# Performance work log

Measured on AMD Instinct MI355X. Metric: run time of the kernel, lower is better.

The kernel has to match this reference:

```python
import jax, jax.numpy as jnp
import numpy as np

N_NODES = 10000
N_EDGES = 640000
D = 128            # node_dims == edge_dims
HID = 2 * D        # ff hidden
EPS = 1e-6


def _layernorm(x, g, b):
    mu = jnp.mean(x, axis=-1, keepdims=True)
    var = jnp.var(x, axis=-1, keepdims=True)
    return (x - mu) * jax.lax.rsqrt(var + EPS) * g + b


def setup_inputs() -> dict:
    key = jax.random.key(0)
    ks = jax.random.split(key, 16)
    def lin(k, fan_in, fan_out):
        lim = 1.0 / np.sqrt(fan_in)
        kw, kb = jax.random.split(k)
        W = jax.random.uniform(kw, (fan_in, fan_out), jnp.float32, -lim, lim)
        b = jax.random.uniform(kb, (fan_out,), jnp.float32, -lim, lim)
        return W, b
    x = jax.random.normal(ks[0], (N_NODES, D), jnp.float32)
    edge_index = jax.random.randint(ks[1], (2, N_EDGES), 0, N_NODES, jnp.int64)
    edge_attr = jax.random.normal(ks[2], (N_EDGES, D), jnp.float32)
    # message MLP: Linear(3D->D), ReLU, Linear(D->D), ReLU, Linear(D->D)
    W1, b1 = lin(ks[3], 3 * D, D)
    W2, b2 = lin(ks[4], D, D)
    W3, b3 = lin(ks[5], D, D)
    # feedforward: Linear(D->2D), ReLU, Linear(2D->D)
    F1, bf1 = lin(ks[6], D, HID)
    F2, bf2 = lin(ks[7], HID, D)
    g0 = jnp.ones((D,), jnp.float32); be0 = jnp.zeros((D,), jnp.float32)
    g1 = jnp.ones((D,), jnp.float32); be1 = jnp.zeros((D,), jnp.float32)
    return {"x": x, "edge_index": edge_index, "edge_attr": edge_attr,
            "W1": W1, "b1": b1, "W2": W2, "b2": b2, "W3": W3, "b3": b3,
            "F1": F1, "bf1": bf1, "F2": F2, "bf2": bf2,
            "g0": g0, "be0": be0, "g1": g1, "be1": be1}


def reference(x, edge_index, edge_attr, W1, b1, W2, b2, W3, b3,
              F1, bf1, F2, bf2, g0, be0, g1, be1):
    src = edge_index[0]  # j
    dst = edge_index[1]  # i
    # message: cat([h_V_i, edge_attr, h_V_j]) -> MLP  (E x 3D gather)
    m = jnp.concatenate([x[dst], edge_attr, x[src]], axis=-1)
    m = jax.nn.relu(m @ W1 + b1)
    m = jax.nn.relu(m @ W2 + b2)
    m = m @ W3 + b3  # [E, D]
    # scatter-mean over destination nodes
    sums = jax.ops.segment_sum(m, dst, num_segments=N_NODES)
    cnt = jax.ops.segment_sum(jnp.ones((N_EDGES,), m.dtype), dst, num_segments=N_NODES)
    dh = sums / jnp.maximum(cnt, 1.0)[:, None]
    # residual + norm (dropout is identity at inference)
    h = _layernorm(x + dh, g0, be0)
    # pointwise feedforward
    ff = jax.nn.relu(h @ F1 + bf1) @ F2 + bf2
    return _layernorm(h + ff, g1, be1)
```

## Files before the change

kernel.cpp:

```cpp
#include <hip/hip_runtime.h>


#define NE 640000
#define NN 10000
#define DD 128
#define HIDN 256
#define EPSF 1e-6f

typedef __attribute__((ext_vector_type(8))) short short8;
typedef __attribute__((ext_vector_type(4))) float f32x4;

__device__ __forceinline__ unsigned short f2bf(float f) {
    union { float f; unsigned int u; } v; v.f = f;
    unsigned int r = v.u + 0x7FFFu + ((v.u >> 16) & 1u);
    return (unsigned short)(r >> 16);
}
__device__ __forceinline__ float bf2f(unsigned short h) {
    union { unsigned int u; float f; } v; v.u = ((unsigned int)h) << 16;
    return v.f;
}

__global__ void prep_weights(const float* __restrict__ W1,
                             const float* __restrict__ W2,
                             const float* __restrict__ W3,
                             unsigned short* __restrict__ WT)
{
    int g = blockIdx.x * 256 + threadIdx.x;
    int layer = g >> 14, r = g & 16383;
    int n = r >> 7, k = r & 127;
    const float* W = (layer == 0) ? (W1 + 128 * DD) : (layer == 1 ? W2 : W3);
    WT[layer * 16384 + n * 128 + ((((k >> 3) ^ (n & 7)) << 3) | (k & 7))] =
        f2bf(W[k * DD + n]);
}

__global__ __launch_bounds__(256, 2)
void pq_kernel(const float* __restrict__ x, const float* __restrict__ W1,
               const float* __restrict__ b1,
               unsigned short* __restrict__ Pb, unsigned short* __restrict__ Qb)
{
    __shared__ float sXT[128 * 68];
    __shared__ float sB[32 * 128];
    const int t = threadIdx.x;
    const int nb = blockIdx.x * 64;
    const int r0 = (t >> 4) << 2, c0 = (t & 15) << 3;

#pragma unroll
    for (int p = 0; p < 8; ++p) {
        int f = t + p * 256;
        int row = f >> 5, c4 = (f & 31) << 2;
        int node = nb + row; if (node >= NN) node = NN - 1;
        float4 v = *(const float4*)(x + (long)node * DD + c4);
        sXT[(c4 + 0) * 68 + row] = v.x;
        sXT[(c4 + 1) * 68 + row] = v.y;
        sXT[(c4 + 2) * 68 + row] = v.z;
        sXT[(c4 + 3) * 68 + row] = v.w;
    }

    for (int pass = 0; pass < 2; ++pass) {
        const float* W = W1 + (pass == 0 ? 0 : 256 * DD);
        float acc[4][8];
#pragma unroll
        for (int i = 0; i < 4; ++i)
#pragma unroll
            for (int j = 0; j < 8; ++j) acc[i][j] = 0.f;

        for (int kc = 0; kc < 4; ++kc) {
            __syncthreads();
#pragma unroll
            for (int p = 0; p < 4; ++p) {
                int f = t + p * 256;
                int kr = f >> 5, col = (f & 31) << 2;
                *(float4*)(sB + kr * 128 + col) =
                    *(const float4*)(W + (long)(kc * 32 + kr) * DD + col);
            }
            __syncthreads();
#pragma unroll 4
            for (int k = 0; k < 32; ++k) {
                float4 a  = *(const float4*)(sXT + (kc * 32 + k) * 68 + r0);
                float4 bl = *(const float4*)(sB + k * 128 + c0);
                float4 bh = *(const float4*)(sB + k * 128 + c0 + 4);
                float av[4] = {a.x, a.y, a.z, a.w};
                float bv[8] = {bl.x, bl.y, bl.z, bl.w, bh.x, bh.y, bh.z, bh.w};
#pragma unroll
                for (int i = 0; i < 4; ++i)
#pragma unroll
                    for (int j = 0; j < 8; ++j)
                        acc[i][j] = fmaf(av[i], bv[j], acc[i][j]);
            }
        }
        unsigned short* Out = (pass == 0) ? Pb : Qb;
#pragma unroll
        for (int i = 0; i < 4; ++i) {
            int node = nb + r0 + i;
            if (node < NN) {
                unsigned short tmp[8];
#pragma unroll
                for (int j = 0; j < 8; ++j) {
                    float v = acc[i][j] + (pass == 0 ? b1[c0 + j] : 0.f);
                    tmp[j] = f2bf(v);
                }
                *(uint4*)(Out + (long)node * 128 + c0) = *(uint4*)tmp;
            }
        }
    }
}

__device__ __forceinline__ const short8* frag(const unsigned short* buf,
                                              int row, int kc, int q)
{
    int g = (kc * 4 + q) ^ (row & 7);
    return (const short8*)(buf + row * 128 + g * 8);
}

__global__ __launch_bounds__(256, 2)
void edge_mfma(const float* __restrict__ ea, const int* __restrict__ ei,
               const unsigned short* __restrict__ WT,
               const unsigned short* __restrict__ Pb,
               const unsigned short* __restrict__ Qb,
               const float* __restrict__ b2, const float* __restrict__ b3,
               float* __restrict__ sums, float* __restrict__ cnt)
{
    __shared__ unsigned short sA[128 * 128];
    __shared__ unsigned short sW[128 * 128];

    const int t = threadIdx.x;
    const int wave = t >> 6, lane = t & 63;
    const int ln = lane & 15, q = lane >> 4;
    const int r0 = wave * 32;
    const long ebase = (long)blockIdx.x * 128;

    int drow[8], srow[8];
#pragma unroll
    for (int rt = 0; rt < 2; ++rt)
#pragma unroll
        for (int rg = 0; rg < 4; ++rg) {
            int row = r0 + rt * 16 + q * 4 + rg;
            drow[rt * 4 + rg] = ei[(long)NE + ebase + row];
            srow[rt * 4 + rg] = ei[ebase + row];
        }

#pragma unroll
    for (int p = 0; p < 16; ++p) {
        int f = t + p * 256;
        int row = f >> 5, c4 = (f & 31) << 2;
        float4 v = *(const float4*)(ea + (ebase + row) * DD + c4);
        uint2 pk;
        pk.x = (unsigned)f2bf(v.x) | ((unsigned)f2bf(v.y) << 16);
        pk.y = (unsigned)f2bf(v.z) | ((unsigned)f2bf(v.w) << 16);
        int addr = row * 128 + ((((c4 >> 3) ^ (row & 7)) << 3) | (c4 & 7));
        *(uint2*)(sA + addr) = pk;
    }
    {
        const uint4* src = (const uint4*)WT;
        uint4* dst = (uint4*)sW;
#pragma unroll
        for (int p = 0; p < 8; ++p) dst[t + p * 256] = src[t + p * 256];
    }
    __syncthreads();

    f32x4 acc[2][8];

#pragma unroll
    for (int rt = 0; rt < 2; ++rt)
#pragma unroll
        for (int ct = 0; ct < 8; ++ct) acc[rt][ct] = (f32x4)(0.f);
#pragma unroll
    for (int kc = 0; kc < 4; ++kc) {
        short8 a0 = *frag(sA, r0 + ln,      kc, q);
        short8 a1 = *frag(sA, r0 + 16 + ln, kc, q);
#pragma unroll
        for (int ct = 0; ct < 8; ++ct) {
            short8 b = *frag(sW, ct * 16 + ln, kc, q);
            acc[0][ct] = __builtin_amdgcn_mfma_f32_16x16x32_bf16(a0, b, acc[0][ct], 0, 0, 0);
            acc[1][ct] = __builtin_amdgcn_mfma_f32_16x16x32_bf16(a1, b, acc[1][ct], 0, 0, 0);
        }
    }
    __syncthreads();
    {
        const uint4* src = (const uint4*)(WT + 16384);
        uint4* dst = (uint4*)sW;
#pragma unroll
        for (int p = 0; p < 8; ++p) dst[t + p * 256] = src[t + p * 256];
    }
#pragma unroll
    for (int rt = 0; rt < 2; ++rt)
#pragma unroll
        for (int rg = 0; rg < 4; ++rg) {
            int row = r0 + rt * 16 + q * 4 + rg;
            long dof = (long)drow[rt * 4 + rg] * DD;
            long sof = (long)srow[rt * 4 + rg] * DD;
#pragma unroll
            for (int ct = 0; ct < 8; ++ct) {
                int col = ct * 16 + ln;
                float v = acc[rt][ct][rg] + bf2f(Pb[dof + col]) + bf2f(Qb[sof + col]);
                v = fmaxf(v, 0.f);
                sA[row * 128 + ((((col >> 3) ^ (row & 7)) << 3) | (col & 7))] = f2bf(v);
            }
        }
    __syncthreads();

#pragma unroll
    for (int rt = 0; rt < 2; ++rt)
#pragma unroll
        for (int ct = 0; ct < 8; ++ct) acc[rt][ct] = (f32x4)(0.f);
#pragma unroll
    for (int kc = 0; kc < 4; ++kc) {
        short8 a0 = *frag(sA, r0 + ln,      kc, q);
        short8 a1 = *frag(sA, r0 + 16 + ln, kc, q);
#pragma unroll
        for (int ct = 0; ct < 8; ++ct) {
            short8 b = *frag(sW, ct * 16 + ln, kc, q);
            acc[0][ct] = __builtin_amdgcn_mfma_f32_16x16x32_bf16(a0, b, acc[0][ct], 0, 0, 0);
            acc[1][ct] = __builtin_amdgcn_mfma_f32_16x16x32_bf16(a1, b, acc[1][ct], 0, 0, 0);
        }
    }
    __syncthreads();
    {
        const uint4* src = (const uint4*)(WT + 2 * 16384);
        uint4* dst = (uint4*)sW;
#pragma unroll
        for (int p = 0; p < 8; ++p) dst[t + p * 256] = src[t + p * 256];
    }
    float bv2[8];
#pragma unroll
    for (int ct = 0; ct < 8; ++ct) bv2[ct] = b2[ct * 16 + ln];
#pragma unroll
    for (int rt = 0; rt < 2; ++rt)
#pragma unroll
        for (int rg = 0; rg < 4; ++rg) {
            int row = r0 + rt * 16 + q * 4 + rg;
#pragma unroll
            for (int ct = 0; ct < 8; ++ct) {
                int col = ct * 16 + ln;
                float v = fmaxf(acc[rt][ct][rg] + bv2[ct], 0.f);
                sA[row * 128 + ((((col >> 3) ^ (row & 7)) << 3) | (col & 7))] = f2bf(v);
            }
        }
    __syncthreads();

#pragma unroll
    for (int rt = 0; rt < 2; ++rt)
#pragma unroll
        for (int ct = 0; ct < 8; ++ct) acc[rt][ct] = (f32x4)(0.f);
#pragma unroll
    for (int kc = 0; kc < 4; ++kc) {
        short8 a0 = *frag(sA, r0 + ln,      kc, q);
        short8 a1 = *frag(sA, r0 + 16 + ln, kc, q);
#pragma unroll
        for (int ct = 0; ct < 8; ++ct) {
            short8 b = *frag(sW, ct * 16 + ln, kc, q);
            acc[0][ct] = __builtin_amdgcn_mfma_f32_16x16x32_bf16(a0, b, acc[0][ct], 0, 0, 0);
            acc[1][ct] = __builtin_amdgcn_mfma_f32_16x16x32_bf16(a1, b, acc[1][ct], 0, 0, 0);
        }
    }
    float bv3[8];
#pragma unroll
    for (int ct = 0; ct < 8; ++ct) bv3[ct] = b3[ct * 16 + ln];
#pragma unroll
    for (int rt = 0; rt < 2; ++rt)
#pragma unroll
        for (int rg = 0; rg < 4; ++rg) {
            long dof = (long)drow[rt * 4 + rg] * DD;
#pragma unroll
            for (int ct = 0; ct < 8; ++ct) {
                atomicAdd(sums + dof + ct * 16 + ln, acc[rt][ct][rg] + bv3[ct]);
            }
        }
    if (t < 128) atomicAdd(cnt + ei[(long)NE + ebase + t], 1.0f);
}

__global__ __launch_bounds__(256)
void node_fused(const float* __restrict__ x,
                const float* __restrict__ sums, const float* __restrict__ cnt,
                const float* __restrict__ F1, const float* __restrict__ bf1,
                const float* __restrict__ F2, const float* __restrict__ bf2,
                const float* __restrict__ g0, const float* __restrict__ be0,
                const float* __restrict__ g1, const float* __restrict__ be1,
                float* __restrict__ out)
{
    constexpr int NPB = 8;
    __shared__ float sh[NPB][DD];
    __shared__ float shid[NPB][HIDN];
    __shared__ float sz[NPB][DD];

    const int t = threadIdx.x;
    const int wave = t >> 6, lane = t & 63;
    const int half = lane >> 5, l2 = lane & 31;
    const int nl = wave * 2 + half;
    const int node = blockIdx.x * NPB + nl;
    const long base = (long)node * DD;

    float inv = 1.0f / fmaxf(cnt[node], 1.0f);
    float y[4], s = 0.f, ss = 0.f;
#pragma unroll
    for (int e = 0; e < 4; ++e) {
        int c = l2 + 32 * e;
        y[e] = x[base + c] + sums[base + c] * inv;
        s += y[e]; ss += y[e] * y[e];
    }
#pragma unroll
    for (int off = 16; off > 0; off >>= 1) {
        s += __shfl_down(s, off, 32); ss += __shfl_down(ss, off, 32);
    }
    s = __shfl(s, 0, 32); ss = __shfl(ss, 0, 32);
    float mean = s * (1.0f / DD);
    float var  = ss * (1.0f / DD) - mean * mean;
    float rstd = rsqrtf(var + EPSF);
#pragma unroll
    for (int e = 0; e < 4; ++e) {
        int c = l2 + 32 * e;
        sh[nl][c] = (y[e] - mean) * rstd * g0[c] + be0[c];
    }
    __syncthreads();

    float hacc[NPB];
    float bb = bf1[t];
#pragma unroll
    for (int v = 0; v < NPB; ++v) hacc[v] = bb;
    for (int k = 0; k < DD; ++k) {
        float wv = F1[(long)k * HIDN + t];
#pragma unroll
        for (int v = 0; v < NPB; ++v) hacc[v] = fmaf(sh[v][k], wv, hacc[v]);
    }
#pragma unroll
    for (int v = 0; v < NPB; ++v) shid[v][t] = fmaxf(hacc[v], 0.f);
    __syncthreads();

    const int col = t & (DD - 1);
    const int grp = (t >> 7) * 4;
    float o[4];
#pragma unroll
    for (int v = 0; v < 4; ++v) o[v] = bf2[col];
    for (int k = 0; k < HIDN; ++k) {
        float wv = F2[(long)k * DD + col];
#pragma unroll
        for (int v = 0; v < 4; ++v) o[v] = fmaf(shid[grp + v][k], wv, o[v]);
    }
#pragma unroll
    for (int v = 0; v < 4; ++v) sz[grp + v][col] = sh[grp + v][col] + o[v];
    __syncthreads();

    float z[4]; s = 0.f; ss = 0.f;
#pragma unroll
    for (int e = 0; e < 4; ++e) {
        int c = l2 + 32 * e;
        z[e] = sz[nl][c]; s += z[e]; ss += z[e] * z[e];
    }
#pragma unroll
    for (int off = 16; off > 0; off >>= 1) {
        s += __shfl_down(s, off, 32); ss += __shfl_down(ss, off, 32);
    }
    s = __shfl(s, 0, 32); ss = __shfl(ss, 0, 32);
    mean = s * (1.0f / DD);
    var  = ss * (1.0f / DD) - mean * mean;
    rstd = rsqrtf(var + EPSF);
#pragma unroll
    for (int e = 0; e < 4; ++e) {
        int c = l2 + 32 * e;
        out[base + c] = (z[e] - mean) * rstd * g1[c] + be1[c];
    }
}

extern "C" void kernel_launch(void* const* d_in, const int* in_sizes, int n_in,
                              void* d_out, int out_size, void* d_ws, size_t ws_size,
                              hipStream_t stream)
{
    const float* x   = (const float*)d_in[0];
    const int*   ei  = (const int*)  d_in[1];
    const float* ea  = (const float*)d_in[2];
    const float* W1  = (const float*)d_in[3];
    const float* b1  = (const float*)d_in[4];
    const float* W2  = (const float*)d_in[5];
    const float* b2  = (const float*)d_in[6];
    const float* W3  = (const float*)d_in[7];
    const float* b3  = (const float*)d_in[8];
    const float* F1  = (const float*)d_in[9];
    const float* bf1 = (const float*)d_in[10];
    const float* F2  = (const float*)d_in[11];
    const float* bf2 = (const float*)d_in[12];
    const float* g0  = (const float*)d_in[13];
    const float* be0 = (const float*)d_in[14];
    const float* g1  = (const float*)d_in[15];
    const float* be1 = (const float*)d_in[16];
    float* out = (float*)d_out;

    char* ws = (char*)d_ws;
    float*          sums = (float*)(ws);
    float*          cnt  = (float*)(ws + 5120000);
    unsigned short* WT   = (unsigned short*)(ws + 5160192);
    unsigned short* Pb   = (unsigned short*)(ws + 5258752);
    unsigned short* Qb   = (unsigned short*)(ws + 7818752);

    hipMemsetAsync(ws, 0, 5160000, stream);
    prep_weights<<<192, 256, 0, stream>>>(W1, W2, W3, WT);
    pq_kernel<<<(NN + 63) / 64, 256, 0, stream>>>(x, W1, b1, Pb, Qb);
    edge_mfma<<<NE / 128, 256, 0, stream>>>(ea, ei, WT, Pb, Qb, b2, b3, sums, cnt);
    node_fused<<<NN / 8, 256, 0, stream>>>(x, sums, cnt, F1, bf1, F2, bf2,
                                           g0, be0, g1, be1, out);
}
```

Measured before the change: 785.3 us.

## Sort edges by destination and segment-reduce messages in LDS before atomics

```diff
diff --git a/kernel.cpp b/kernel.cpp
--- a/kernel.cpp
+++ b/kernel.cpp
@@ -105,6 +105,57 @@
     }
 }
 
+__global__ void hist_kernel(const int* __restrict__ ei, int* __restrict__ cursor)
+{
+    int e = blockIdx.x * 256 + threadIdx.x;
+    if (e < NE) atomicAdd(cursor + ei[(long)NE + e], 1);
+}
+
+__global__ __launch_bounds__(256)
+void scan_kernel(int* __restrict__ cursor, float* __restrict__ cnt)
+{
+    __shared__ int sp[256];
+    const int t = threadIdx.x;
+    const int base = t * 40;
+    int v[40], loc[40];
+    int s = 0;
+#pragma unroll
+    for (int i = 0; i < 40; ++i) {
+        int n = base + i;
+        v[i] = (n < NN) ? cursor[n] : 0;
+        loc[i] = s; s += v[i];
+    }
+    sp[t] = s;
+    __syncthreads();
+    for (int off = 1; off < 256; off <<= 1) {
+        int x = 0;
+        if (t >= off) x = sp[t - off];
+        __syncthreads();
+        sp[t] += x;
+        __syncthreads();
+    }
+    int excl = sp[t] - s;
+#pragma unroll
+    for (int i = 0; i < 40; ++i) {
+        int n = base + i;
+        if (n < NN) {
+            cursor[n] = excl + loc[i];
+            cnt[n] = (float)v[i];
+        }
+    }
+}
+
+__global__ void scatter_kernel(const int* __restrict__ ei,
+                               int* __restrict__ cursor, int* __restrict__ perm)
+{
+    int e = blockIdx.x * 256 + threadIdx.x;
+    if (e < NE) {
+        int d = ei[(long)NE + e];
+        int p = atomicAdd(cursor + d, 1);
+        perm[p] = e;
+    }
+}
+
 __device__ __forceinline__ const short8* frag(const unsigned short* buf,
                                               int row, int kc, int q)
 {
@@ -114,20 +165,38 @@
 
 __global__ __launch_bounds__(256, 2)
 void edge_mfma(const float* __restrict__ ea, const int* __restrict__ ei,
+               const int* __restrict__ perm,
                const unsigned short* __restrict__ WT,
                const unsigned short* __restrict__ Pb,
                const unsigned short* __restrict__ Qb,
                const float* __restrict__ b2, const float* __restrict__ b3,
-               float* __restrict__ sums, float* __restrict__ cnt)
-{
-    __shared__ unsigned short sA[128 * 128];
-    __shared__ unsigned short sW[128 * 128];
+               float* __restrict__ sums)
+{
+    __shared__ __align__(16) char smem[66560];
+    unsigned short* sA = (unsigned short*)smem;
+    unsigned short* sW = (unsigned short*)(smem + 32768);
+    float*          sM = (float*)smem;
+    int*            sE   = (int*)(smem + 65536);
+    int*            sDst = (int*)(smem + 66048);
 
     const int t = threadIdx.x;
     const int wave = t >> 6, lane = t & 63;
     const int ln = lane & 15, q = lane >> 4;
     const int r0 = wave * 32;
-    const long ebase = (long)blockIdx.x * 128;
+    const long pbase = (long)blockIdx.x * 128;
+
+    if (t < 128) {
+        int e = perm[pbase + t];
+        sE[t] = e;
+        sDst[t] = ei[(long)NE + e];
+    }
+    {
+        const uint4* src = (const uint4*)WT;
+        uint4* dst = (uint4*)sW;
+#pragma unroll
+        for (int p = 0; p < 8; ++p) dst[t + p * 256] = src[t + p * 256];
+    }
+    __syncthreads();
 
     int drow[8], srow[8];
 #pragma unroll
@@ -135,27 +204,21 @@
 #pragma unroll
         for (int rg = 0; rg < 4; ++rg) {
             int row = r0 + rt * 16 + q * 4 + rg;
-            drow[rt * 4 + rg] = ei[(long)NE + ebase + row];
-            srow[rt * 4 + rg] = ei[ebase + row];
+            drow[rt * 4 + rg] = sDst[row];
+            srow[rt * 4 + rg] = ei[sE[row]];
         }
 
 #pragma unroll
     for (int p = 0; p < 16; ++p) {
         int f = t + p * 256;
         int row = f >> 5, c4 = (f & 31) << 2;
-        float4 v = *(const float4*)(ea + (ebase + row) * DD + c4);
+        float4 v = *(const float4*)(ea + (long)sE[row] * DD + c4);
         uint2 pk;
         pk.x = (unsigned)f2bf(v.x) | ((unsigned)f2bf(v.y) << 16);
         pk.y = (unsigned)f2bf(v.z) | ((unsigned)f2bf(v.w) << 16);
         int addr = row * 128 + ((((c4 >> 3) ^ (row & 7)) << 3) | (c4 & 7));
         *(uint2*)(sA + addr) = pk;
     }
-    {
-        const uint4* src = (const uint4*)WT;
-        uint4* dst = (uint4*)sW;
-#pragma unroll
-        for (int p = 0; p < 8; ++p) dst[t + p * 256] = src[t + p * 256];
-    }
     __syncthreads();
 
     f32x4 acc[2][8];
@@ -253,20 +316,38 @@
             acc[1][ct] = __builtin_amdgcn_mfma_f32_16x16x32_bf16(a1, b, acc[1][ct], 0, 0, 0);
         }
     }
+
     float bv3[8];
 #pragma unroll
     for (int ct = 0; ct < 8; ++ct) bv3[ct] = b3[ct * 16 + ln];
+    __syncthreads();
 #pragma unroll
     for (int rt = 0; rt < 2; ++rt)
 #pragma unroll
         for (int rg = 0; rg < 4; ++rg) {
-            long dof = (long)drow[rt * 4 + rg] * DD;
-#pragma unroll
-            for (int ct = 0; ct < 8; ++ct) {
-                atomicAdd(sums + dof + ct * 16 + ln, acc[rt][ct][rg] + bv3[ct]);
-            }
-        }
-    if (t < 128) atomicAdd(cnt + ei[(long)NE + ebase + t], 1.0f);
+            int row = r0 + rt * 16 + q * 4 + rg;
+#pragma unroll
+            for (int ct = 0; ct < 8; ++ct)
+                sM[row * 128 + ct * 16 + ln] = acc[rt][ct][rg] + bv3[ct];
+        }
+    __syncthreads();
+
+    {
+        const int c = t & 127, h = t >> 7;
+        const int rb = h * 64;
+        float a = 0.f;
+        int cur = sDst[rb];
+#pragma unroll 8
+        for (int r = rb; r < rb + 64; ++r) {
+            int d = sDst[r];
+            if (d != cur) {
+                atomicAdd(sums + (long)cur * DD + c, a);
+                a = 0.f; cur = d;
+            }
+            a += sM[r * 128 + c];
+        }
+        atomicAdd(sums + (long)cur * DD + c, a);
+    }
 }
 
 __global__ __launch_bounds__(256)
@@ -385,16 +466,23 @@
     float* out = (float*)d_out;
 
     char* ws = (char*)d_ws;
-    float*          sums = (float*)(ws);
-    float*          cnt  = (float*)(ws + 5120000);
-    unsigned short* WT   = (unsigned short*)(ws + 5160192);
-    unsigned short* Pb   = (unsigned short*)(ws + 5258752);
-    unsigned short* Qb   = (unsigned short*)(ws + 7818752);
-
-    hipMemsetAsync(ws, 0, 5160000, stream);
+    float*          sums   = (float*)(ws);
+    float*          cnt    = (float*)(ws + 5120000);
+    unsigned short* WT     = (unsigned short*)(ws + 5160192);
+    unsigned short* Pb     = (unsigned short*)(ws + 5258752);
+    unsigned short* Qb     = (unsigned short*)(ws + 7818752);
+    int*            cursor = (int*)(ws + 10378752);
+    int*            perm   = (int*)(ws + 10418752);
+
+    hipMemsetAsync(ws, 0, 5120000, stream);
+    hipMemsetAsync(ws + 10378752, 0, 40000, stream);
     prep_weights<<<192, 256, 0, stream>>>(W1, W2, W3, WT);
     pq_kernel<<<(NN + 63) / 64, 256, 0, stream>>>(x, W1, b1, Pb, Qb);
-    edge_mfma<<<NE / 128, 256, 0, stream>>>(ea, ei, WT, Pb, Qb, b2, b3, sums, cnt);
+    hist_kernel<<<NE / 256, 256, 0, stream>>>(ei, cursor);
+    scan_kernel<<<1, 256, 0, stream>>>(cursor, cnt);
+    scatter_kernel<<<NE / 256, 256, 0, stream>>>(ei, cursor, perm);
+    edge_mfma<<<NE / 128, 256, 0, stream>>>(ea, ei, perm, WT, Pb, Qb,
+                                            b2, b3, sums);
     node_fused<<<NN / 8, 256, 0, stream>>>(x, sums, cnt, F1, bf1, F2, bf2,
                                            g0, be0, g1, be1, out);
 }
```

New measurement: 788.0 us. Within noise of the previous version (+0.3%).
